# Performance work log

Measured on AMD Instinct MI355X. Metric: run time of the kernel, lower is better.

The kernel has to match this reference:

```python
import jax, jax.numpy as jnp
import numpy as np

B, C, H, W = 16, 512, 32, 32
HW = H * W  # == input_features == output_features for shapes to be consistent


def setup_inputs() -> dict:
    key = jax.random.key(0)
    k1, k2, k3 = jax.random.split(key, 3)
    node1 = jax.random.normal(k1, (B, C, H, W), dtype=jnp.float32)
    node2 = jax.random.normal(k2, (B, C, H, W), dtype=jnp.float32)
    # nn.Linear(input_features, output_features, bias=False).weight: [out, in]
    W_c = jax.random.normal(k3, (HW, HW), dtype=jnp.float32) * (1.0 / np.sqrt(HW))
    return {"node1": node1, "node2": node2, "W_c": W_c}


def reference(node1, node2, W_c):
    b, c, h, w = node1.shape
    hw = h * w
    n1 = node1.reshape(b, c, hw)  # [B, C, HW]
    n2 = node2.reshape(b, c, hw)  # [B, C, HW]
    # x = W_c(n1): Linear applies y = x @ W^T  -> [B, C, HW_out]
    x = jnp.einsum('bch,oh->bco', n1, W_c)
    # e = bmm(x.permute(0,2,1), n2): [B, HW_out, C] @ [B, C, HW] -> [B, HW_out, HW]
    e = jnp.einsum('bco,bch->boh', x, n2)
    a = jax.nn.softmax(e, axis=-1)  # softmax over last dim (HW of node2)
    # m = bmm(n2, a): [B, C, HW] @ [B, HW, HW] -> [B, C, HW]
    m = jnp.einsum('bck,bkj->bcj', n2, a)
    return m
```

## Files before the change

kernel.cpp:

```cpp
#include <hip/hip_runtime.h>
#include <math.h>


typedef _Float16 f16;
typedef _Float16 f16x8 __attribute__((ext_vector_type(8)));
typedef _Float16 f16x4 __attribute__((ext_vector_type(4)));
typedef float f32x4 __attribute__((ext_vector_type(4)));

#define L2E 1.442695040888963f

#define WG_BARRIER() asm volatile("s_waitcnt lgkmcnt(0)\ns_barrier" ::: "memory")

__global__ __launch_bounds__(256) void prep(const float* __restrict__ n1,
                                            const float* __restrict__ Wc,
                                            const float* __restrict__ n2,
                                            f16* __restrict__ n1f, f16* __restrict__ Wf,
                                            f16* __restrict__ n2f, f16* __restrict__ n2t) {
    const int bid = blockIdx.x, tid = threadIdx.x;
    if (bid < 4608) {
        const float* s = (bid < 4096) ? n1 : Wc;
        f16* d = (bid < 4096) ? n1f : Wf;
        const size_t i = ((size_t)(bid < 4096 ? bid : bid - 4096) * 256 + tid) * 8;
        f32x4 a = *(const f32x4*)(s + i);
        f32x4 b = *(const f32x4*)(s + i + 4);
        f16x8 o;
        o[0] = (f16)a[0]; o[1] = (f16)a[1]; o[2] = (f16)a[2]; o[3] = (f16)a[3];
        o[4] = (f16)b[0]; o[5] = (f16)b[1]; o[6] = (f16)b[2]; o[7] = (f16)b[3];
        *(f16x8*)(d + i) = o;
        return;
    }
    const int id = bid - 4608;
    const int b = id >> 7;
    const int ry = (id & 127) >> 4;
    const int cx = id & 15;
    const float* S = n2 + (size_t)b * 512 * 1024;
    f16* Dn = n2f + (size_t)b * 512 * 1024;
    f16* Dt = n2t + (size_t)b * 1024 * 512;
    __shared__ f16 Ts[64 * 72];
    const int r0 = ry * 64, c0 = cx * 64;
    const int rr = tid >> 3, cc8 = (tid & 7) * 8;
#pragma unroll
    for (int h = 0; h < 2; ++h) {
        const int row = r0 + rr + 32 * h;
        const float* s = S + (size_t)row * 1024 + c0 + cc8;
        f32x4 a = *(const f32x4*)s, bq = *(const f32x4*)(s + 4);
        f16x8 o;
        o[0] = (f16)a[0]; o[1] = (f16)a[1]; o[2] = (f16)a[2]; o[3] = (f16)a[3];
        o[4] = (f16)bq[0]; o[5] = (f16)bq[1]; o[6] = (f16)bq[2]; o[7] = (f16)bq[3];
        *(f16x8*)&Ts[(rr + 32 * h) * 72 + cc8] = o;
        *(f16x8*)(Dn + (size_t)row * 1024 + c0 + cc8) = o;
    }
    __syncthreads();
    const int j = tid >> 2, k16 = (tid & 3) * 16;
    f16* d = Dt + (size_t)(c0 + j) * 512 + r0 + k16;
    f16x8 o0, o1;
#pragma unroll
    for (int i = 0; i < 8; ++i) {
        o0[i] = Ts[(k16 + i) * 72 + j];
        o1[i] = Ts[(k16 + 8 + i) * 72 + j];
    }
    *(f16x8*)d = o0;
    *(f16x8*)(d + 8) = o1;
}

__global__ __launch_bounds__(256) void stats_combine(const float* __restrict__ Pm,
                                                     const float* __restrict__ Ps,
                                                     float* __restrict__ Sc) {
    const int g = blockIdx.x * 256 + threadIdx.x;
    const int b = g >> 10, o = g & 1023;
    const int mt = o >> 7, ml = o & 127;
    const float* pm = Pm + ((size_t)(b * 8 + mt) * 16) * 128 + ml;
    const float* ps = Ps + ((size_t)(b * 8 + mt) * 16) * 128 + ml;
    float M = -3.0e38f;
#pragma unroll
    for (int p = 0; p < 16; ++p) M = fmaxf(M, pm[p * 128]);
    float S = 0.f;
#pragma unroll
    for (int p = 0; p < 16; ++p) S += ps[p * 128] * exp2f(pm[p * 128] - M);
    Sc[g] = M + __log2f(S);
}

__device__ __forceinline__ f16x8 expb(f16x8 b, f32x4 cl, f32x4 ch) {
    f16x8 t;
#pragma unroll
    for (int i = 0; i < 4; ++i) t[i] = (f16)exp2f(fmaf((float)b[i], L2E, -cl[i]));
#pragma unroll
    for (int i = 0; i < 4; ++i) t[4 + i] = (f16)exp2f(fmaf((float)b[4 + i], L2E, -ch[i]));
    return t;
}

template <int NS, bool EXPB>
__device__ __forceinline__ void gemm_core128(const char* gA, const char* gB,
                                             const float* gS, char* SM,
                                             int sOff0, int sOff1,
                                             int wm, int wn, int col, int swz16,
                                             f32x4 (&acc)[4][4]) {
    f32x4 c0a, c0b, c0c, c0d, c1a, c1b, c1c, c1d;
    f16x8 pa0 = *(const f16x8*)gA, pa1 = *(const f16x8*)(gA + 16);
    f16x8 pb0 = *(const f16x8*)gB, pb1 = *(const f16x8*)(gB + 16);
    if (EXPB) {
        c0a = *(const f32x4*)gS;        c0b = *(const f32x4*)(gS + 4);
        c0c = *(const f32x4*)(gS + 8);  c0d = *(const f32x4*)(gS + 12);
    }
    *(f16x8*)(SM + sOff0) = pa0;
    *(f16x8*)(SM + sOff1) = pa1;
    *(f16x8*)(SM + 16384 + sOff0) = EXPB ? expb(pb0, c0a, c0b) : pb0;
    *(f16x8*)(SM + 16384 + sOff1) = EXPB ? expb(pb1, c0c, c0d) : pb1;
    f16x8 qa0 = *(const f16x8*)(gA + 64), qa1 = *(const f16x8*)(gA + 80);
    f16x8 qb0 = *(const f16x8*)(gB + 64), qb1 = *(const f16x8*)(gB + 80);
    if (EXPB) {
        c1a = *(const f32x4*)(gS + 32); c1b = *(const f32x4*)(gS + 36);
        c1c = *(const f32x4*)(gS + 40); c1d = *(const f32x4*)(gS + 44);
    }
    pa0 = *(const f16x8*)(gA + 128); pa1 = *(const f16x8*)(gA + 144);
    pb0 = *(const f16x8*)(gB + 128); pb1 = *(const f16x8*)(gB + 144);
    if (EXPB) {
        c0a = *(const f32x4*)(gS + 64); c0b = *(const f32x4*)(gS + 68);
        c0c = *(const f32x4*)(gS + 72); c0d = *(const f32x4*)(gS + 76);
    }
    WG_BARRIER();
#pragma unroll
    for (int kb = 0; kb < NS; ++kb) {
        const char* Ac = SM + (kb & 1) * 8192;
        const char* Bc = SM + 16384 + (kb & 1) * 8192;
        f16x8 fa[4], fb[4];
#pragma unroll
        for (int u = 0; u < 4; ++u)
            fa[u] = *(const f16x8*)(Ac + (wm + u * 16 + col) * 64 + swz16);
#pragma unroll
        for (int v = 0; v < 4; ++v)
            fb[v] = *(const f16x8*)(Bc + (wn + v * 16 + col) * 64 + swz16);
#pragma unroll
        for (int u = 0; u < 4; ++u)
#pragma unroll
            for (int v = 0; v < 4; ++v)
                acc[u][v] = __builtin_amdgcn_mfma_f32_16x16x32_f16(fa[u], fb[v],
                                                                   acc[u][v], 0, 0, 0);
        if (kb + 1 < NS) {
            char* dA = SM + ((kb + 1) & 1) * 8192;
            char* dB = SM + 16384 + ((kb + 1) & 1) * 8192;
            if ((kb & 1) == 0) {
                *(f16x8*)(dA + sOff0) = qa0;
                *(f16x8*)(dA + sOff1) = qa1;
                *(f16x8*)(dB + sOff0) = EXPB ? expb(qb0, c1a, c1b) : qb0;
                *(f16x8*)(dB + sOff1) = EXPB ? expb(qb1, c1c, c1d) : qb1;
                if (kb + 3 < NS) {
                    qa0 = *(const f16x8*)(gA + (size_t)(kb + 3) * 64);
                    qa1 = *(const f16x8*)(gA + (size_t)(kb + 3) * 64 + 16);
                    qb0 = *(const f16x8*)(gB + (size_t)(kb + 3) * 64);
                    qb1 = *(const f16x8*)(gB + (size_t)(kb + 3) * 64 + 16);
                    if (EXPB) {
                        c1a = *(const f32x4*)(gS + (size_t)(kb + 3) * 32);
                        c1b = *(const f32x4*)(gS + (size_t)(kb + 3) * 32 + 4);
                        c1c = *(const f32x4*)(gS + (size_t)(kb + 3) * 32 + 8);
                        c1d = *(const f32x4*)(gS + (size_t)(kb + 3) * 32 + 12);
                    }
                }
            } else {
                *(f16x8*)(dA + sOff0) = pa0;
                *(f16x8*)(dA + sOff1) = pa1;
                *(f16x8*)(dB + sOff0) = EXPB ? expb(pb0, c0a, c0b) : pb0;
                *(f16x8*)(dB + sOff1) = EXPB ? expb(pb1, c0c, c0d) : pb1;
                if (kb + 3 < NS) {
                    pa0 = *(const f16x8*)(gA + (size_t)(kb + 3) * 64);
                    pa1 = *(const f16x8*)(gA + (size_t)(kb + 3) * 64 + 16);
                    pb0 = *(const f16x8*)(gB + (size_t)(kb + 3) * 64);
                    pb1 = *(const f16x8*)(gB + (size_t)(kb + 3) * 64 + 16);
                    if (EXPB) {
                        c0a = *(const f32x4*)(gS + (size_t)(kb + 3) * 32);
                        c0b = *(const f32x4*)(gS + (size_t)(kb + 3) * 32 + 4);
                        c0c = *(const f32x4*)(gS + (size_t)(kb + 3) * 32 + 8);
                        c0d = *(const f32x4*)(gS + (size_t)(kb + 3) * 32 + 12);
                    }
                }
            }
            WG_BARRIER();
        }
    }
}

__device__ __forceinline__ void epilogue_tr128(f32x4 (&acc)[4][4], char* SM,
                                               f16* dst0, int dstRow, int m0,
                                               int n0, int tid) {
    const int lane = tid & 63, wave = tid >> 6;
    const int col = lane & 15, quad = lane >> 4;
    const int wm = ((wave >> 1) & 1) * 64, wn = (wave & 1) * 64;
    WG_BARRIER();
    f16* Tt = (f16*)SM;
#pragma unroll
    for (int u = 0; u < 4; ++u)
#pragma unroll
        for (int v = 0; v < 4; ++v) {
            f16x4 p;
#pragma unroll
            for (int r = 0; r < 4; ++r) p[r] = (f16)acc[u][v][r];
            *(f16x4*)&Tt[(wn + v * 16 + col) * 136 + wm + u * 16 + quad * 4] = p;
        }
    WG_BARRIER();
    const int j = tid >> 1, seg = (tid & 1) * 64;
    f16* dst = dst0 + (size_t)(n0 + j) * dstRow + m0 + seg;
#pragma unroll
    for (int c8 = 0; c8 < 64; c8 += 8)
        *(f16x8*)(dst + c8) = *(const f16x8*)&Tt[j * 136 + seg + c8];
}

__global__ __launch_bounds__(256) void gemm1_nt_xt(const f16* __restrict__ A,
                                                   const f16* __restrict__ Bw,
                                                   f16* __restrict__ Xt) {
    const int K = 1024;
    const int id = blockIdx.x;
    const int xcd = id & 7, loc = id >> 3;
    const int b = xcd * 2 + (loc >> 5);
    const int m0 = ((loc >> 3) & 3) * 128;
    const int n0 = (loc & 7) * 128;
    A += (size_t)b * 512 * K;
    Xt += (size_t)b * 1024 * 512;
    __shared__ __attribute__((aligned(16))) char SM[34816];
    const int tid = threadIdx.x, lane = tid & 63, wave = tid >> 6;
    const int col = lane & 15, quad = lane >> 4;
    const int wm = ((wave >> 1) & 1) * 64, wn = (wave & 1) * 64;
    const int srow = tid >> 1, spair = (tid & 1) * 2;
    const int sx = (srow >> 1) & 3;
    const int sOff0 = srow * 64 + ((spair ^ sx) * 16);
    const int sOff1 = srow * 64 + (((spair + 1) ^ sx) * 16);
    const int swz16 = (quad ^ ((col >> 1) & 3)) * 16;
    const char* gA = (const char*)A + (size_t)(m0 + srow) * K * 2 + spair * 16;
    const char* gB = (const char*)Bw + (size_t)(n0 + srow) * K * 2 + spair * 16;
    f32x4 acc[4][4] = {};
    gemm_core128<32, false>(gA, gB, nullptr, SM, sOff0, sOff1, wm, wn, col, swz16, acc);
    epilogue_tr128(acc, SM, Xt, 512, m0, n0, tid);
}

__global__ __launch_bounds__(256) void gemm2_nt_et(const f16* __restrict__ A,
                                                   const f16* __restrict__ B,
                                                   f16* __restrict__ Et,
                                                   float* __restrict__ Pm,
                                                   float* __restrict__ Ps) {
    const int K = 512;
    const int id = blockIdx.x;
    const int xcd = id & 7, loc = id >> 3;
    const int b = xcd * 2 + (loc >> 6);
    const int m0 = ((loc >> 3) & 7) * 128;
    const int n0 = (loc & 7) * 128;
    A += (size_t)b * 1024 * K;
    B += (size_t)b * 1024 * K;
    Et += (size_t)b * 1024 * 1024;
    __shared__ __attribute__((aligned(16))) char SM[34816];
    const int tid = threadIdx.x, lane = tid & 63, wave = tid >> 6;
    const int col = lane & 15, quad = lane >> 4;
    const int wm = ((wave >> 1) & 1) * 64, wn = (wave & 1) * 64;
    const int srow = tid >> 1, spair = (tid & 1) * 2;
    const int sx = (srow >> 1) & 3;
    const int sOff0 = srow * 64 + ((spair ^ sx) * 16);
    const int sOff1 = srow * 64 + (((spair + 1) ^ sx) * 16);
    const int swz16 = (quad ^ ((col >> 1) & 3)) * 16;
    const char* gA = (const char*)A + (size_t)(m0 + srow) * K * 2 + spair * 16;
    const char* gB = (const char*)B + (size_t)(n0 + srow) * K * 2 + spair * 16;
    f32x4 acc[4][4] = {};
    gemm_core128<16, false>(gA, gB, nullptr, SM, sOff0, sOff1, wm, wn, col, swz16, acc);

    {
        float pm[16], ps[16];
#pragma unroll
        for (int u = 0; u < 4; ++u)
#pragma unroll
            for (int r = 0; r < 4; ++r) {
                float w0 = (float)(f16)acc[u][0][r] * L2E;
                float w1 = (float)(f16)acc[u][1][r] * L2E;
                float w2 = (float)(f16)acc[u][2][r] * L2E;
                float w3 = (float)(f16)acc[u][3][r] * L2E;
                float m2 = fmaxf(fmaxf(w0, w1), fmaxf(w2, w3));
                float s = exp2f(w0 - m2) + exp2f(w1 - m2) +
                          exp2f(w2 - m2) + exp2f(w3 - m2);
                pm[u * 4 + r] = m2;
                ps[u * 4 + r] = s;
            }
#pragma unroll
        for (int d = 1; d < 16; d <<= 1)
#pragma unroll
            for (int i = 0; i < 16; ++i) {
                float om = __shfl_xor(pm[i], d, 64);
                float os = __shfl_xor(ps[i], d, 64);
                float nm = fmaxf(pm[i], om);
                ps[i] = ps[i] * exp2f(pm[i] - nm) + os * exp2f(om - nm);
                pm[i] = nm;
            }
        if (col == 0) {
            const int part = ((b * 8 + (m0 >> 7)) * 8 + (n0 >> 7)) * 2 + (wave & 1);
            float* bm = Pm + (size_t)part * 128;
            float* bs = Ps + (size_t)part * 128;
#pragma unroll
            for (int i = 0; i < 16; ++i) {
                const int ml = wm + (i >> 2) * 16 + quad * 4 + (i & 3);
                bm[ml] = pm[i];
                bs[ml] = ps[i];
            }
        }
    }

    epilogue_tr128(acc, SM, Et, 1024, m0, n0, tid);
}

__global__ __launch_bounds__(256) void gemm3_nt_out(const f16* __restrict__ A,
                                                    const f16* __restrict__ Et,
                                                    const float* __restrict__ Sc,
                                                    float* __restrict__ C) {
    const int K = 1024;
    const int id = blockIdx.x;
    const int xcd = id & 7, loc = id >> 3;
    const int b = xcd * 2 + (loc >> 5);
    const int m0 = ((loc >> 3) & 3) * 128;
    const int n0 = (loc & 7) * 128;
    A += (size_t)b * 512 * K;
    Et += (size_t)b * 1024 * K;
    Sc += (size_t)b * 1024;
    C += (size_t)b * 512 * 1024;
    __shared__ __attribute__((aligned(16))) char SM[34816];
    const int tid = threadIdx.x, lane = tid & 63, wave = tid >> 6;
    const int col = lane & 15, quad = lane >> 4;
    const int wm = ((wave >> 1) & 1) * 64, wn = (wave & 1) * 64;
    const int srow = tid >> 1, spair = (tid & 1) * 2;
    const int sx = (srow >> 1) & 3;
    const int sOff0 = srow * 64 + ((spair ^ sx) * 16);
    const int sOff1 = srow * 64 + (((spair + 1) ^ sx) * 16);
    const int swz16 = (quad ^ ((col >> 1) & 3)) * 16;
    const char* gA = (const char*)A + (size_t)(m0 + srow) * K * 2 + spair * 16;
    const char* gB = (const char*)Et + (size_t)(n0 + srow) * K * 2 + spair * 16;
    const float* gS = Sc + spair * 8;
    f32x4 acc[4][4] = {};
    gemm_core128<32, true>(gA, gB, gS, SM, sOff0, sOff1, wm, wn, col, swz16, acc);

#pragma unroll
    for (int u = 0; u < 4; ++u)
#pragma unroll
        for (int v = 0; v < 4; ++v)
#pragma unroll
            for (int r = 0; r < 4; ++r)
                C[(size_t)(m0 + wm + u * 16 + quad * 4 + r) * 1024 + n0 + wn + v * 16 + col] =
                    acc[u][v][r];
}

extern "C" void kernel_launch(void* const* d_in, const int* in_sizes, int n_in,
                              void* d_out, int out_size, void* d_ws, size_t ws_size,
                              hipStream_t stream) {
    const float* n1 = (const float*)d_in[0];
    const float* n2 = (const float*)d_in[1];
    const float* Wc = (const float*)d_in[2];
    float* out = (float*)d_out;
    char* ws = (char*)d_ws;

    f16* n2t = (f16*)(ws);
    f16* Xt  = (f16*)(ws + (16u << 20));
    f16* Wf  = (f16*)(ws + (32u << 20));
    f16* Et  = (f16*)(ws + (32u << 20));
    f16* n1f = (f16*)(ws + (64u << 20));
    f16* n2f = (f16*)(ws + (80u << 20));
    float* Pm = (float*)(ws + (64u << 20));
    float* Ps = (float*)(ws + (65u << 20));
    float* Sc = (float*)(ws + (66u << 20));

    prep<<<6656, dim3(256), 0, stream>>>(n1, Wc, n2, n1f, Wf, n2f, n2t);
    gemm1_nt_xt<<<512, dim3(256), 0, stream>>>(n1f, Wf, Xt);
    gemm2_nt_et<<<1024, dim3(256), 0, stream>>>(Xt, n2t, Et, Pm, Ps);
    stats_combine<<<64, dim3(256), 0, stream>>>(Pm, Ps, Sc);
    gemm3_nt_out<<<512, dim3(256), 0, stream>>>(n2f, Et, Sc, out);
}
```

Before: 233.8 us.

## Use direct global-to-LDS DMA loads in GEMMs and split softmax exp into separate kernel

```diff
diff --git a/kernel.cpp b/kernel.cpp
--- a/kernel.cpp
+++ b/kernel.cpp
@@ -9,7 +9,10 @@
 
 #define L2E 1.442695040888963f
 
-#define WG_BARRIER() asm volatile("s_waitcnt lgkmcnt(0)\ns_barrier" ::: "memory")
+#define DMA16(g, l)                                                             \
+    __builtin_amdgcn_global_load_lds(                                           \
+        (const __attribute__((address_space(1))) void*)(g),                     \
+        (__attribute__((address_space(3))) void*)(l), 16, 0, 0)
 
 __global__ __launch_bounds__(256) void prep(const float* __restrict__ n1,
                                             const float* __restrict__ Wc,
@@ -89,38 +92,45 @@
     return t;
 }
 
-template <int NS, bool EXPB>
-__device__ __forceinline__ void gemm_core128(const char* gA, const char* gB,
-                                             const float* gS, char* SM,
-                                             int sOff0, int sOff1,
-                                             int wm, int wn, int col, int swz16,
-                                             f32x4 (&acc)[4][4]) {
-    f32x4 c0a, c0b, c0c, c0d, c1a, c1b, c1c, c1d;
-    f16x8 pa0 = *(const f16x8*)gA, pa1 = *(const f16x8*)(gA + 16);
-    f16x8 pb0 = *(const f16x8*)gB, pb1 = *(const f16x8*)(gB + 16);
-    if (EXPB) {
-        c0a = *(const f32x4*)gS;        c0b = *(const f32x4*)(gS + 4);
-        c0c = *(const f32x4*)(gS + 8);  c0d = *(const f32x4*)(gS + 12);
-    }
-    *(f16x8*)(SM + sOff0) = pa0;
-    *(f16x8*)(SM + sOff1) = pa1;
-    *(f16x8*)(SM + 16384 + sOff0) = EXPB ? expb(pb0, c0a, c0b) : pb0;
-    *(f16x8*)(SM + 16384 + sOff1) = EXPB ? expb(pb1, c0c, c0d) : pb1;
-    f16x8 qa0 = *(const f16x8*)(gA + 64), qa1 = *(const f16x8*)(gA + 80);
-    f16x8 qb0 = *(const f16x8*)(gB + 64), qb1 = *(const f16x8*)(gB + 80);
-    if (EXPB) {
-        c1a = *(const f32x4*)(gS + 32); c1b = *(const f32x4*)(gS + 36);
-        c1c = *(const f32x4*)(gS + 40); c1d = *(const f32x4*)(gS + 44);
-    }
-    pa0 = *(const f16x8*)(gA + 128); pa1 = *(const f16x8*)(gA + 144);
-    pb0 = *(const f16x8*)(gB + 128); pb1 = *(const f16x8*)(gB + 144);
-    if (EXPB) {
-        c0a = *(const f32x4*)(gS + 64); c0b = *(const f32x4*)(gS + 68);
-        c0c = *(const f32x4*)(gS + 72); c0d = *(const f32x4*)(gS + 76);
-    }
-    WG_BARRIER();
+__global__ __launch_bounds__(256) void at_scale(const f16* __restrict__ Et,
+                                                const float* __restrict__ Sc,
+                                                f16* __restrict__ At) {
+    const int gid = blockIdx.x;
+    const int b = gid >> 9;
+    const int row = (gid & 511) * 2 + (threadIdx.x >> 7);
+    const int ch = threadIdx.x & 127;
+    const size_t base = ((size_t)b << 20) + ((size_t)row << 10) + ch * 8;
+    const float* sc = Sc + (b << 10) + ch * 8;
+    f16x8 v = *(const f16x8*)(Et + base);
+    f32x4 c0 = *(const f32x4*)sc, c1 = *(const f32x4*)(sc + 4);
+    *(f16x8*)(At + base) = expb(v, c0, c1);
+}
+
+template <int NS>
+__device__ __forceinline__ void gemm_dma(const char* gA, const char* gB,
+                                         const int ldK, char* SM, int tid,
+                                         int wm, int wn, int col, int swz16,
+                                         f32x4 (&acc)[4][4]) {
+    const int r = tid >> 2, ls = tid & 3;
+    const int x = (r >> 1) & 3;
+    const char* sA0 = gA + (size_t)r * ldK + (ls ^ x) * 16;
+    const char* sA1 = sA0 + (size_t)64 * ldK;
+    const char* sB0 = gB + (size_t)r * ldK + (ls ^ x) * 16;
+    const char* sB1 = sB0 + (size_t)64 * ldK;
+    const int wave = tid >> 6;
+    char* dA = SM + wave * 1024;
+    char* dB = SM + 16384 + wave * 1024;
+    DMA16(sA0, dA); DMA16(sA1, dA + 4096);
+    DMA16(sB0, dB); DMA16(sB1, dB + 4096);
+    __syncthreads();
 #pragma unroll
     for (int kb = 0; kb < NS; ++kb) {
+        if (kb + 1 < NS) {
+            const int nb = ((kb + 1) & 1) * 8192;
+            const int o = (kb + 1) * 64;
+            DMA16(sA0 + o, dA + nb); DMA16(sA1 + o, dA + nb + 4096);
+            DMA16(sB0 + o, dB + nb); DMA16(sB1 + o, dB + nb + 4096);
+        }
         const char* Ac = SM + (kb & 1) * 8192;
         const char* Bc = SM + 16384 + (kb & 1) * 8192;
         f16x8 fa[4], fb[4];
@@ -136,46 +146,7 @@
             for (int v = 0; v < 4; ++v)
                 acc[u][v] = __builtin_amdgcn_mfma_f32_16x16x32_f16(fa[u], fb[v],
                                                                    acc[u][v], 0, 0, 0);
-        if (kb + 1 < NS) {
-            char* dA = SM + ((kb + 1) & 1) * 8192;
-            char* dB = SM + 16384 + ((kb + 1) & 1) * 8192;
-            if ((kb & 1) == 0) {
-                *(f16x8*)(dA + sOff0) = qa0;
-                *(f16x8*)(dA + sOff1) = qa1;
-                *(f16x8*)(dB + sOff0) = EXPB ? expb(qb0, c1a, c1b) : qb0;
-                *(f16x8*)(dB + sOff1) = EXPB ? expb(qb1, c1c, c1d) : qb1;
-                if (kb + 3 < NS) {
-                    qa0 = *(const f16x8*)(gA + (size_t)(kb + 3) * 64);
-                    qa1 = *(const f16x8*)(gA + (size_t)(kb + 3) * 64 + 16);
-                    qb0 = *(const f16x8*)(gB + (size_t)(kb + 3) * 64);
-                    qb1 = *(const f16x8*)(gB + (size_t)(kb + 3) * 64 + 16);
-                    if (EXPB) {
-                        c1a = *(const f32x4*)(gS + (size_t)(kb + 3) * 32);
-                        c1b = *(const f32x4*)(gS + (size_t)(kb + 3) * 32 + 4);
-                        c1c = *(const f32x4*)(gS + (size_t)(kb + 3) * 32 + 8);
-                        c1d = *(const f32x4*)(gS + (size_t)(kb + 3) * 32 + 12);
-                    }
-                }
-            } else {
-                *(f16x8*)(dA + sOff0) = pa0;
-                *(f16x8*)(dA + sOff1) = pa1;
-                *(f16x8*)(dB + sOff0) = EXPB ? expb(pb0, c0a, c0b) : pb0;
-                *(f16x8*)(dB + sOff1) = EXPB ? expb(pb1, c0c, c0d) : pb1;
-                if (kb + 3 < NS) {
-                    pa0 = *(const f16x8*)(gA + (size_t)(kb + 3) * 64);
-                    pa1 = *(const f16x8*)(gA + (size_t)(kb + 3) * 64 + 16);
-                    pb0 = *(const f16x8*)(gB + (size_t)(kb + 3) * 64);
-                    pb1 = *(const f16x8*)(gB + (size_t)(kb + 3) * 64 + 16);
-                    if (EXPB) {
-                        c0a = *(const f32x4*)(gS + (size_t)(kb + 3) * 32);
-                        c0b = *(const f32x4*)(gS + (size_t)(kb + 3) * 32 + 4);
-                        c0c = *(const f32x4*)(gS + (size_t)(kb + 3) * 32 + 8);
-                        c0d = *(const f32x4*)(gS + (size_t)(kb + 3) * 32 + 12);
-                    }
-                }
-            }
-            WG_BARRIER();
-        }
+        __syncthreads();
     }
 }
 
@@ -185,7 +156,6 @@
     const int lane = tid & 63, wave = tid >> 6;
     const int col = lane & 15, quad = lane >> 4;
     const int wm = ((wave >> 1) & 1) * 64, wn = (wave & 1) * 64;
-    WG_BARRIER();
     f16* Tt = (f16*)SM;
 #pragma unroll
     for (int u = 0; u < 4; ++u)
@@ -196,7 +166,7 @@
             for (int r = 0; r < 4; ++r) p[r] = (f16)acc[u][v][r];
             *(f16x4*)&Tt[(wn + v * 16 + col) * 136 + wm + u * 16 + quad * 4] = p;
         }
-    WG_BARRIER();
+    __syncthreads();
     const int j = tid >> 1, seg = (tid & 1) * 64;
     f16* dst = dst0 + (size_t)(n0 + j) * dstRow + m0 + seg;
 #pragma unroll
@@ -207,28 +177,21 @@
 __global__ __launch_bounds__(256) void gemm1_nt_xt(const f16* __restrict__ A,
                                                    const f16* __restrict__ Bw,
                                                    f16* __restrict__ Xt) {
-    const int K = 1024;
     const int id = blockIdx.x;
     const int xcd = id & 7, loc = id >> 3;
     const int b = xcd * 2 + (loc >> 5);
     const int m0 = ((loc >> 3) & 3) * 128;
     const int n0 = (loc & 7) * 128;
-    A += (size_t)b * 512 * K;
-    Xt += (size_t)b * 1024 * 512;
     __shared__ __attribute__((aligned(16))) char SM[34816];
     const int tid = threadIdx.x, lane = tid & 63, wave = tid >> 6;
     const int col = lane & 15, quad = lane >> 4;
     const int wm = ((wave >> 1) & 1) * 64, wn = (wave & 1) * 64;
-    const int srow = tid >> 1, spair = (tid & 1) * 2;
-    const int sx = (srow >> 1) & 3;
-    const int sOff0 = srow * 64 + ((spair ^ sx) * 16);
-    const int sOff1 = srow * 64 + (((spair + 1) ^ sx) * 16);
     const int swz16 = (quad ^ ((col >> 1) & 3)) * 16;
-    const char* gA = (const char*)A + (size_t)(m0 + srow) * K * 2 + spair * 16;
-    const char* gB = (const char*)Bw + (size_t)(n0 + srow) * K * 2 + spair * 16;
+    const char* gA = (const char*)(A + (size_t)b * 512 * 1024) + (size_t)m0 * 2048;
+    const char* gB = (const char*)(Bw) + (size_t)n0 * 2048;
     f32x4 acc[4][4] = {};
-    gemm_core128<32, false>(gA, gB, nullptr, SM, sOff0, sOff1, wm, wn, col, swz16, acc);
-    epilogue_tr128(acc, SM, Xt, 512, m0, n0, tid);
+    gemm_dma<32>(gA, gB, 2048, SM, tid, wm, wn, col, swz16, acc);
+    epilogue_tr128(acc, SM, Xt + (size_t)b * 1024 * 512, 512, m0, n0, tid);
 }
 
 __global__ __launch_bounds__(256) void gemm2_nt_et(const f16* __restrict__ A,
@@ -236,28 +199,20 @@
                                                    f16* __restrict__ Et,
                                                    float* __restrict__ Pm,
                                                    float* __restrict__ Ps) {
-    const int K = 512;
     const int id = blockIdx.x;
     const int xcd = id & 7, loc = id >> 3;
     const int b = xcd * 2 + (loc >> 6);
     const int m0 = ((loc >> 3) & 7) * 128;
     const int n0 = (loc & 7) * 128;
-    A += (size_t)b * 1024 * K;
-    B += (size_t)b * 1024 * K;
-    Et += (size_t)b * 1024 * 1024;
     __shared__ __attribute__((aligned(16))) char SM[34816];
     const int tid = threadIdx.x, lane = tid & 63, wave = tid >> 6;
     const int col = lane & 15, quad = lane >> 4;
     const int wm = ((wave >> 1) & 1) * 64, wn = (wave & 1) * 64;
-    const int srow = tid >> 1, spair = (tid & 1) * 2;
-    const int sx = (srow >> 1) & 3;
-    const int sOff0 = srow * 64 + ((spair ^ sx) * 16);
-    const int sOff1 = srow * 64 + (((spair + 1) ^ sx) * 16);
     const int swz16 = (quad ^ ((col >> 1) & 3)) * 16;
-    const char* gA = (const char*)A + (size_t)(m0 + srow) * K * 2 + spair * 16;
-    const char* gB = (const char*)B + (size_t)(n0 + srow) * K * 2 + spair * 16;
+    const char* gA = (const char*)(A + (size_t)b * 1024 * 512) + (size_t)m0 * 1024;
+    const char* gB = (const char*)(B + (size_t)b * 1024 * 512) + (size_t)n0 * 1024;
     f32x4 acc[4][4] = {};
-    gemm_core128<16, false>(gA, gB, nullptr, SM, sOff0, sOff1, wm, wn, col, swz16, acc);
+    gemm_dma<16>(gA, gB, 1024, SM, tid, wm, wn, col, swz16, acc);
 
     {
         float pm[16], ps[16];
@@ -298,37 +253,27 @@
         }
     }
 
-    epilogue_tr128(acc, SM, Et, 1024, m0, n0, tid);
+    epilogue_tr128(acc, SM, Et + (size_t)b * 1024 * 1024, 1024, m0, n0, tid);
 }
 
 __global__ __launch_bounds__(256) void gemm3_nt_out(const f16* __restrict__ A,
-                                                    const f16* __restrict__ Et,
-                                                    const float* __restrict__ Sc,
+                                                    const f16* __restrict__ At,
                                                     float* __restrict__ C) {
-    const int K = 1024;
     const int id = blockIdx.x;
     const int xcd = id & 7, loc = id >> 3;
     const int b = xcd * 2 + (loc >> 5);
     const int m0 = ((loc >> 3) & 3) * 128;
     const int n0 = (loc & 7) * 128;
-    A += (size_t)b * 512 * K;
-    Et += (size_t)b * 1024 * K;
-    Sc += (size_t)b * 1024;
     C += (size_t)b * 512 * 1024;
-    __shared__ __attribute__((aligned(16))) char SM[34816];
+    __shared__ __attribute__((aligned(16))) char SM[32768];
     const int tid = threadIdx.x, lane = tid & 63, wave = tid >> 6;
     const int col = lane & 15, quad = lane >> 4;
     const int wm = ((wave >> 1) & 1) * 64, wn = (wave & 1) * 64;
-    const int srow = tid >> 1, spair = (tid & 1) * 2;
-    const int sx = (srow >> 1) & 3;
-    const int sOff0 = srow * 64 + ((spair ^ sx) * 16);
-    const int sOff1 = srow * 64 + (((spair + 1) ^ sx) * 16);
     const int swz16 = (quad ^ ((col >> 1) & 3)) * 16;
-    const char* gA = (const char*)A + (size_t)(m0 + srow) * K * 2 + spair * 16;
-    const char* gB = (const char*)Et + (size_t)(n0 + srow) * K * 2 + spair * 16;
-    const float* gS = Sc + spair * 8;
+    const char* gA = (const char*)(A + (size_t)b * 512 * 1024) + (size_t)m0 * 2048;
+    const char* gB = (const char*)(At + (size_t)b * 1024 * 1024) + (size_t)n0 * 2048;
     f32x4 acc[4][4] = {};
-    gemm_core128<32, true>(gA, gB, gS, SM, sOff0, sOff1, wm, wn, col, swz16, acc);
+    gemm_dma<32>(gA, gB, 2048, SM, tid, wm, wn, col, swz16, acc);
 
 #pragma unroll
     for (int u = 0; u < 4; ++u)
@@ -351,6 +296,7 @@
 
     f16* n2t = (f16*)(ws);
     f16* Xt  = (f16*)(ws + (16u << 20));
+    f16* At  = (f16*)(ws);
     f16* Wf  = (f16*)(ws + (32u << 20));
     f16* Et  = (f16*)(ws + (32u << 20));
     f16* n1f = (f16*)(ws + (64u << 20));
@@ -363,5 +309,6 @@
     gemm1_nt_xt<<<512, dim3(256), 0, stream>>>(n1f, Wf, Xt);
     gemm2_nt_et<<<1024, dim3(256), 0, stream>>>(Xt, n2t, Et, Pm, Ps);
     stats_combine<<<64, dim3(256), 0, stream>>>(Pm, Ps, Sc);
-    gemm3_nt_out<<<512, dim3(256), 0, stream>>>(n2f, Et, Sc, out);
-}
+    at_scale<<<8192, dim3(256), 0, stream>>>(Et, Sc, At);
+    gemm3_nt_out<<<512, dim3(256), 0, stream>>>(n2f, At, out);
+}
```

Result: no change. 234.0 us (+0.1%).
